# Kernel optimization log

Hardware: AMD Instinct MI355X
Metric: run time of the kernel (lower is better)

The kernel has to match this reference:

```python
import jax, jax.numpy as jnp
import numpy as np

N = 50000   # nodes
E = 200000  # triplets
IN = 128    # num_in_features
H = 4       # heads
F = 64      # num_out_features
HID = 64    # attention_mlp_hidden


def setup_inputs() -> dict:
    key = jax.random.key(0)
    ks = jax.random.split(key, 12)
    rn = lambda k, shape, s=0.05: (jax.random.normal(k, shape, jnp.float32) * s)
    return {
        "in_nodes_features": jax.random.normal(ks[0], (N, IN), jnp.float32),
        "edge_index": jax.random.randint(ks[1], (3, E), 0, N, jnp.int32),
        "W_proj": rn(ks[2], (H * F, IN)),          # linear_proj (no bias)
        "att_W1": rn(ks[3], (HID, 3 * F)),
        "att_b1": jnp.zeros((HID,), jnp.float32),
        "att_W2": rn(ks[4], (1, HID)),
        "att_b2": jnp.zeros((1,), jnp.float32),
        "e_W1": rn(ks[5], (F, 2 * F)),
        "e_b1": jnp.zeros((F,), jnp.float32),
        "e_W2": rn(ks[6], (F, F)),
        "e_b2": jnp.zeros((F,), jnp.float32),
        "theta": rn(ks[7], (1, H, F), 0.1),
        "bias": jnp.zeros((H * F,), jnp.float32),
    }


def _edge_nn(pair, e_W1, e_b1, e_W2, e_b2):
    # pair: [E, H, 2F] -> [E, H, F]
    h = jax.nn.leaky_relu(jnp.einsum('ehc,fc->ehf', pair, e_W1) + e_b1, 0.2)
    return jnp.einsum('ehf,gf->ehg', h, e_W2) + e_b2


def reference(in_nodes_features, edge_index, W_proj, att_W1, att_b1, att_W2,
              att_b2, e_W1, e_b1, e_W2, e_b2, theta, bias):
    proj = (in_nodes_features @ W_proj.T).reshape(-1, H, F)  # [N, H, F]
    pi = proj[edge_index[0]]  # [E, H, F]
    pj = proj[edge_index[1]]
    pk = proj[edge_index[2]]

    # attention MLP on concatenated triplet features
    comb = jnp.concatenate([pi, pj, pk], axis=-1)            # [E, H, 3F]
    h = jax.nn.relu(jnp.einsum('ehc,dc->ehd', comb, att_W1) + att_b1)
    scores = (jnp.einsum('ehd,od->eho', h, att_W2) + att_b2)[..., 0]  # [E, H]
    scores = jax.nn.leaky_relu(scores, 0.2)
    att = jax.nn.softmax(scores, axis=-1)[..., None]         # softmax over heads, [E, H, 1]

    pairs = [(pj, pk), (pi, pk), (pi, pj)]
    outs = []
    for i in range(3):
        prod = _edge_nn(jnp.concatenate(pairs[i], axis=-1), e_W1, e_b1, e_W2, e_b2)
        ws = jax.ops.segment_sum(att * prod, edge_index[i], num_segments=proj.shape[0])
        outs.append(theta * proj + ws)                       # [N, H, F]

    out = jnp.concatenate(outs, axis=0).reshape(-1, H * F)   # [3N, H*F]
    out = out + bias
    return jax.nn.elu(out)
```

## Files before the change

kernel.cpp:

```cpp
#include <hip/hip_runtime.h>
#include <hip/hip_bf16.h>

#define N_NODES 50000
#define N_EDGES 200000
#define IN_F 128
#define HEADS 4
#define FD 64
#define HF 256
#define NCOLS 1536
#define NT3 (3 * N_NODES)
#define E3  (3 * N_EDGES)
#define TROW 320

#define OFF_PROJ   0UL
#define OFF_TABS   51200000UL
#define OFF_ATT    179200000UL
#define OFF_RANK   182400000UL
#define OFF_ELIST2 184800000UL
#define OFF_CNT    194400000UL
#define OFF_OFFS   195000000UL
#define OFF_BSUM   195600008UL
#define OFF_BSW    195601040UL
#define OFF_CB     195994256UL

typedef __attribute__((ext_vector_type(8))) short short8;
typedef __attribute__((ext_vector_type(4))) float f32x4;

__device__ inline short bf16_of(float x) {
    __hip_bfloat16 h = __float2bfloat16(x);
    return *reinterpret_cast<short*>(&h);
}
__device__ inline unsigned pack2(float lo, float hi) {
    return ((unsigned)(unsigned short)bf16_of(hi) << 16) |
           (unsigned)(unsigned short)bf16_of(lo);
}
__device__ inline short8 pack8(float4 a, float4 b) {
    short8 o;
    o[0] = bf16_of(a.x); o[1] = bf16_of(a.y); o[2] = bf16_of(a.z); o[3] = bf16_of(a.w);
    o[4] = bf16_of(b.x); o[5] = bf16_of(b.y); o[6] = bf16_of(b.z); o[7] = bf16_of(b.w);
    return o;
}
__device__ inline void unpk(uint4 v, float* f) {
    f[0] = __uint_as_float(v.x << 16); f[1] = __uint_as_float(v.x & 0xffff0000u);
    f[2] = __uint_as_float(v.y << 16); f[3] = __uint_as_float(v.y & 0xffff0000u);
    f[4] = __uint_as_float(v.z << 16); f[5] = __uint_as_float(v.z & 0xffff0000u);
    f[6] = __uint_as_float(v.w << 16); f[7] = __uint_as_float(v.w & 0xffff0000u);
}
__device__ inline float score8(uint4 ua, uint4 ub, uint4 uc, const float* w) {
    float fa[8], fb[8], fc[8]; unpk(ua, fa); unpk(ub, fb); unpk(uc, fc);
    float p = 0.f;
#pragma unroll
    for (int j = 0; j < 8; ++j) {
        float x = fa[j] + fb[j] + fc[j];
        x = fmaxf(x, 0.f);
        p = fmaf(x, w[j], p);
    }
    return p;
}

__global__ __launch_bounds__(128) void k_comp(const float* __restrict__ Wp,
                                              const float* __restrict__ attW1,
                                              const float* __restrict__ eW1,
                                              const float* __restrict__ attb1,
                                              const float* __restrict__ eb1,
                                              __hip_bfloat16* __restrict__ Bsw,
                                              float* __restrict__ colbias) {
    const int c = blockIdx.x;
    const int k = threadIdx.x;
    float acc;
    float cb = 0.f;
    if (c < HF) {
        acc = Wp[c * IN_F + k];
    } else {
        const int t = (c - HF) >> 8;
        const int rem = (c - HF) & 255;
        const int h = rem >> 6, g = rem & 63;
        const float* T;
        if (t == 0)      T = attW1 + g * 192;
        else if (t == 1) T = attW1 + g * 192 + 64;
        else if (t == 2) T = attW1 + g * 192 + 128;
        else if (t == 3) T = eW1 + g * 128;
        else             T = eW1 + g * 128 + 64;
        acc = 0.f;
        for (int f = 0; f < 64; ++f)
            acc += T[f] * Wp[(h * 64 + f) * IN_F + k];
        if (t == 0) cb = attb1[g];
        else if (t == 3) cb = eb1[g];
    }
    const int ct = c >> 4, cin = c & 15, kin = k & 31, j = k & 7;
    const int ks = k >> 5;
    const int l = cin + ((kin >> 3) << 4);
    Bsw[((ct * 4 + ks) * 64 + l) * 8 + j] = __float2bfloat16(acc);
    if (k == 0) colbias[c] = cb;
}

__global__ __launch_bounds__(256) void k_tab(const float* __restrict__ in,
                                             const __hip_bfloat16* __restrict__ BswH,
                                             const float* __restrict__ colbias,
                                             float* __restrict__ proj,
                                             __hip_bfloat16* __restrict__ tabs) {
    const short8* Bsw = reinterpret_cast<const short8*>(BswH);
    const int lane = threadIdx.x & 63;
    const int wv = threadIdx.x >> 6;
    const int r = lane & 15, q = lane >> 4;
    const int row0 = blockIdx.x * 16;

    short8 a[4];
    const float* ip = in + (size_t)(row0 + r) * IN_F + q * 8;
#pragma unroll
    for (int ks = 0; ks < 4; ++ks)
        a[ks] = pack8(*(const float4*)(ip + ks * 32), *(const float4*)(ip + ks * 32 + 4));

    for (int ctl = 0; ctl < 24; ++ctl) {
        const int ct = wv * 24 + ctl;
        const int c = ct * 16 + r;
        const float cb = colbias[c];
        f32x4 acc = {cb, cb, cb, cb};
#pragma unroll
        for (int ks = 0; ks < 4; ++ks)
            acc = __builtin_amdgcn_mfma_f32_16x16x32_bf16(a[ks], Bsw[(ct * 4 + ks) * 64 + lane], acc, 0, 0, 0);
        if (c < HF) {
#pragma unroll
            for (int i = 0; i < 4; ++i)
                proj[(size_t)(row0 + q * 4 + i) * HF + c] = acc[i];
        } else {
            const int t = (c - HF) >> 8;
            const int rem = (c - HF) & 255;
            const int h = rem >> 6, g = rem & 63;
#pragma unroll
            for (int i = 0; i < 4; ++i)
                tabs[(((size_t)(row0 + q * 4 + i) * HEADS + h) * 5 + t) * 64 + g] =
                    __float2bfloat16(acc[i]);
        }
    }
}

__global__ __launch_bounds__(256) void k_hist(const int* __restrict__ eidx,
                                              int* __restrict__ cnt,
                                              int* __restrict__ rank) {
    const int g = blockIdx.x * 256 + threadIdx.x;
    if (g < E3) {
        const int node = eidx[g];
        const int t = g / N_EDGES;
        rank[g] = atomicAdd(&cnt[t * N_NODES + node], 1);
    }
}

__global__ __launch_bounds__(256) void k_scan1(const int* __restrict__ cnt,
                                               int* __restrict__ offs,
                                               int* __restrict__ bsums) {
    __shared__ int lds[256];
    const int b = blockIdx.x, t = threadIdx.x;
    const int base = b * 1024 + t * 4;
    int v[4];
#pragma unroll
    for (int c = 0; c < 4; ++c) v[c] = (base + c < NT3) ? cnt[base + c] : 0;
    const int s = v[0] + v[1] + v[2] + v[3];
    lds[t] = s;
    __syncthreads();
    for (int off = 1; off < 256; off <<= 1) {
        int x = (t >= off) ? lds[t - off] : 0;
        __syncthreads();
        lds[t] += x;
        __syncthreads();
    }
    if (t == 255) bsums[b] = lds[255];
    int run = lds[t] - s;
#pragma unroll
    for (int c = 0; c < 4; ++c) {
        if (base + c < NT3) offs[base + c] = run;
        run += v[c];
    }
}

__global__ __launch_bounds__(256) void k_scan2(int* __restrict__ bsums, int nb) {
    __shared__ int lds[256];
    const int t = threadIdx.x;
    const int v = (t < nb) ? bsums[t] : 0;
    lds[t] = v;
    __syncthreads();
    for (int off = 1; off < 256; off <<= 1) {
        int x = (t >= off) ? lds[t - off] : 0;
        __syncthreads();
        lds[t] += x;
        __syncthreads();
    }
    if (t < nb) bsums[t] = lds[t] - v;
}

__global__ __launch_bounds__(256) void k_scan3(int* __restrict__ offs,
                                               const int* __restrict__ bsums) {
    const int i = blockIdx.x * 256 + threadIdx.x;
    if (i < NT3) offs[i] += bsums[i >> 10];
    if (i == NT3) offs[NT3] = E3;
}

__global__ __launch_bounds__(256) void k_scat(const int* __restrict__ eidx,
                                              const int* __restrict__ offs,
                                              const int* __restrict__ rank,
                                              int4* __restrict__ elist2) {
    const int g = blockIdx.x * 256 + threadIdx.x;
    if (g < E3) {
        const int node = eidx[g];
        const int t = g / N_EDGES;
        const int e = g - t * N_EDGES;
        const int s0 = (t == 0) ? 1 : 0;
        const int s1 = (t == 2) ? 1 : 2;
        const int x = eidx[s0 * N_EDGES + e];
        const int y = eidx[s1 * N_EDGES + e];
        elist2[offs[t * N_NODES + node] + rank[g]] = make_int4(x, y, e, 0);
    }
}

__global__ __launch_bounds__(256) void k_att(
        const int* __restrict__ eidx,
        const __hip_bfloat16* __restrict__ tabs,
        const float* __restrict__ attW2, const float* __restrict__ attb2,
        float* __restrict__ attbuf) {
    __shared__ float s_lds[HEADS][16];
    const int lane = threadIdx.x & 63;
    const int h = threadIdx.x >> 6;
    const int r = lane & 15, q = lane >> 4;
    const int e0 = blockIdx.x * 16;

    float awlo[8], awhi[8];
    {
        float4 w0 = *(const float4*)(attW2 + q * 8);
        float4 w1 = *(const float4*)(attW2 + q * 8 + 4);
        awlo[0] = w0.x; awlo[1] = w0.y; awlo[2] = w0.z; awlo[3] = w0.w;
        awlo[4] = w1.x; awlo[5] = w1.y; awlo[6] = w1.z; awlo[7] = w1.w;
        float4 w2 = *(const float4*)(attW2 + 32 + q * 8);
        float4 w3 = *(const float4*)(attW2 + 32 + q * 8 + 4);
        awhi[0] = w2.x; awhi[1] = w2.y; awhi[2] = w2.z; awhi[3] = w2.w;
        awhi[4] = w3.x; awhi[5] = w3.y; awhi[6] = w3.z; awhi[7] = w3.w;
    }
    const float ab2s = attb2[0];

    const int ni = eidx[e0 + r];
    const int nj = eidx[N_EDGES + e0 + r];
    const int nk = eidx[2 * N_EDGES + e0 + r];

    const size_t bi = ((size_t)ni * HEADS + h) * TROW + q * 8;
    const size_t bj = ((size_t)nj * HEADS + h) * TROW + q * 8;
    const size_t bk = ((size_t)nk * HEADS + h) * TROW + q * 8;

    uint4 a0 = *(const uint4*)(tabs + bi);
    uint4 a1 = *(const uint4*)(tabs + bi + 32);
    uint4 b0 = *(const uint4*)(tabs + bj + 64);
    uint4 b1 = *(const uint4*)(tabs + bj + 96);
    uint4 c0 = *(const uint4*)(tabs + bk + 128);
    uint4 c1 = *(const uint4*)(tabs + bk + 160);

    float p = score8(a0, b0, c0, awlo) + score8(a1, b1, c1, awhi);
    p += __shfl_xor(p, 16);
    p += __shfl_xor(p, 32);
    float sc = p + ab2s;
    sc = fmaxf(sc, 0.2f * sc);
    if (lane < 16) s_lds[h][lane] = sc;
    __syncthreads();
    if (lane < 16) {
        const float s0 = s_lds[0][lane], s1 = s_lds[1][lane];
        const float s2 = s_lds[2][lane], s3 = s_lds[3][lane];
        const float mx = fmaxf(fmaxf(s0, s1), fmaxf(s2, s3));
        const float x0 = __expf(s0 - mx), x1 = __expf(s1 - mx);
        const float x2 = __expf(s2 - mx), x3 = __expf(s3 - mx);
        const float rs = 1.f / (x0 + x1 + x2 + x3);
        const float xh = (h == 0) ? x0 : (h == 1) ? x1 : (h == 2) ? x2 : x3;
        attbuf[(size_t)(e0 + lane) * 4 + h] = xh * rs;
    }
}

__global__ __launch_bounds__(256) void k_seg(const int* __restrict__ offs,
                                             const int4* __restrict__ elist2,
                                             const float* __restrict__ attbuf,
                                             const __hip_bfloat16* __restrict__ tabs,
                                             const float* __restrict__ proj,
                                             const float* __restrict__ eW2,
                                             const float* __restrict__ eb2,
                                             const float* __restrict__ theta,
                                             const float* __restrict__ bias,
                                             float* __restrict__ out) {
    __shared__ __hip_bfloat16 S_lds[16][72];
    __shared__ float a_lds[16];
    __shared__ float D_lds[16][68];

    const int lane = threadIdx.x & 63;
    const int w = threadIdx.x >> 6;
    const int h = lane >> 4, r = lane & 15;
    const int q = lane >> 4;
    const int t = blockIdx.y;
    const int n0 = blockIdx.x * 4;
    const int n = n0 + w;
    const int idx = t * N_NODES + n;
    const int p0 = offs[idx], p1 = offs[idx + 1];

    const int c1 = h * TROW + 192 + r * 4;
    const int c2 = h * TROW + 256 + r * 4;

    float acc0 = 0.f, acc1 = 0.f, acc2 = 0.f, acc3 = 0.f, alpha = 0.f;
    for (int base = p0; base < p1; base += 4) {
        int4 exy[4];
#pragma unroll
        for (int c = 0; c < 4; ++c) {
            const int p = base + c;
            exy[c] = elist2[p < p1 ? p : p1 - 1];
        }
        float at[4];
#pragma unroll
        for (int c = 0; c < 4; ++c)
            at[c] = (base + c < p1) ? attbuf[(size_t)exy[c].z * 4 + h] : 0.f;
        uint2 ua[4], ub[4];
#pragma unroll
        for (int c = 0; c < 4; ++c) {
            ua[c] = *(const uint2*)(tabs + ((size_t)exy[c].x * 1280 + c1));
            ub[c] = *(const uint2*)(tabs + ((size_t)exy[c].y * 1280 + c2));
        }
#pragma unroll
        for (int c = 0; c < 4; ++c) {
            float g0 = __uint_as_float(ua[c].x << 16) + __uint_as_float(ub[c].x << 16);
            float g1 = __uint_as_float(ua[c].x & 0xffff0000u) + __uint_as_float(ub[c].x & 0xffff0000u);
            float g2 = __uint_as_float(ua[c].y << 16) + __uint_as_float(ub[c].y << 16);
            float g3 = __uint_as_float(ua[c].y & 0xffff0000u) + __uint_as_float(ub[c].y & 0xffff0000u);
            g0 = fmaxf(g0, 0.2f * g0); g1 = fmaxf(g1, 0.2f * g1);
            g2 = fmaxf(g2, 0.2f * g2); g3 = fmaxf(g3, 0.2f * g3);
            acc0 = fmaf(at[c], g0, acc0); acc1 = fmaf(at[c], g1, acc1);
            acc2 = fmaf(at[c], g2, acc2); acc3 = fmaf(at[c], g3, acc3);
            alpha += at[c];
        }
    }
    const int tr = w * 4 + h;
    uint2 st;
    st.x = pack2(acc0, acc1);
    st.y = pack2(acc2, acc3);
    *(uint2*)&S_lds[tr][r * 4] = st;
    if (r == 0) a_lds[tr] = alpha;
    __syncthreads();

    {
        const float* wp0 = eW2 + (w * 16 + r) * FD + q * 8;
        const float* wp1 = eW2 + (w * 16 + r) * FD + 32 + q * 8;
        short8 bfr0 = pack8(*(const float4*)wp0, *(const float4*)(wp0 + 4));
        short8 bfr1 = pack8(*(const float4*)wp1, *(const float4*)(wp1 + 4));
        short8 A0 = *(short8*)&S_lds[r][q * 8];
        short8 A1 = *(short8*)&S_lds[r][32 + q * 8];
        f32x4 acc = {0.f, 0.f, 0.f, 0.f};
        acc = __builtin_amdgcn_mfma_f32_16x16x32_bf16(A0, bfr0, acc, 0, 0, 0);
        acc = __builtin_amdgcn_mfma_f32_16x16x32_bf16(A1, bfr1, acc, 0, 0, 0);
#pragma unroll
        for (int i = 0; i < 4; ++i)
            D_lds[q * 4 + i][w * 16 + r] = acc[i];
    }
    __syncthreads();

    const int row = threadIdx.x >> 4;
    const int c4 = threadIdx.x & 15;
    const int f = c4 * 4;
    const int hh = row & 3;
    const int nn = n0 + (row >> 2);
    const size_t rho = ((size_t)t * N_NODES + nn) * 4 + hh;

    float4 Dv = *(float4*)&D_lds[row][f];
    float4 pj = *(const float4*)(proj + (size_t)nn * HF + hh * 64 + f);
    float4 th = *(const float4*)(theta + hh * 64 + f);
    float4 bi = *(const float4*)(bias + hh * 64 + f);
    float4 b2 = *(const float4*)(eb2 + f);
    const float al = a_lds[row];
    float4 o;
    float v;
    v = th.x * pj.x + Dv.x + al * b2.x + bi.x; o.x = v > 0.f ? v : expm1f(v);
    v = th.y * pj.y + Dv.y + al * b2.y + bi.y; o.y = v > 0.f ? v : expm1f(v);
    v = th.z * pj.z + Dv.z + al * b2.z + bi.z; o.z = v > 0.f ? v : expm1f(v);
    v = th.w * pj.w + Dv.w + al * b2.w + bi.w; o.w = v > 0.f ? v : expm1f(v);
    *(float4*)(out + rho * 64 + f) = o;
}

extern "C" void kernel_launch(void* const* d_in, const int* in_sizes, int n_in,
                              void* d_out, int out_size, void* d_ws, size_t ws_size,
                              hipStream_t stream) {
    const float* in_nodes = (const float*)d_in[0];
    const int*   eidx     = (const int*)d_in[1];
    const float* Wp       = (const float*)d_in[2];
    const float* attW1    = (const float*)d_in[3];
    const float* attb1    = (const float*)d_in[4];
    const float* attW2    = (const float*)d_in[5];
    const float* attb2    = (const float*)d_in[6];
    const float* eW1      = (const float*)d_in[7];
    const float* eb1      = (const float*)d_in[8];
    const float* eW2      = (const float*)d_in[9];
    const float* eb2      = (const float*)d_in[10];
    const float* theta    = (const float*)d_in[11];
    const float* bias     = (const float*)d_in[12];

    char* ws = (char*)d_ws;
    float*          proj     = (float*)(ws + OFF_PROJ);
    __hip_bfloat16* tabs     = (__hip_bfloat16*)(ws + OFF_TABS);
    float*          attbuf   = (float*)(ws + OFF_ATT);
    int*            rank     = (int*)(ws + OFF_RANK);
    int4*           elist2   = (int4*)(ws + OFF_ELIST2);
    int*            cnt      = (int*)(ws + OFF_CNT);
    int*            offs     = (int*)(ws + OFF_OFFS);
    int*            bsums    = (int*)(ws + OFF_BSUM);
    __hip_bfloat16* Bsw      = (__hip_bfloat16*)(ws + OFF_BSW);
    float*          colbias  = (float*)(ws + OFF_CB);

    float* out = (float*)d_out;

    (void)hipMemsetAsync(cnt, 0, NT3 * sizeof(int), stream);

    k_comp<<<NCOLS, 128, 0, stream>>>(Wp, attW1, eW1, attb1, eb1, Bsw, colbias);
    k_tab<<<N_NODES / 16, 256, 0, stream>>>(in_nodes, Bsw, colbias, proj, tabs);

    k_hist<<<(E3 + 255) / 256, 256, 0, stream>>>(eidx, cnt, rank);
    k_scan1<<<(NT3 + 1023) / 1024, 256, 0, stream>>>(cnt, offs, bsums);
    k_scan2<<<1, 256, 0, stream>>>(bsums, (NT3 + 1023) / 1024);
    k_scan3<<<(NT3 + 256) / 256, 256, 0, stream>>>(offs, bsums);
    k_scat<<<(E3 + 255) / 256, 256, 0, stream>>>(eidx, offs, rank, elist2);

    k_att<<<N_EDGES / 16, 256, 0, stream>>>(eidx, tabs, attW2, attb2, attbuf);
    k_seg<<<dim3(N_NODES / 4, 3), 256, 0, stream>>>(offs, elist2, attbuf,
                                                    tabs, proj, eW2, eb2,
                                                    theta, bias, out);
}
```

Measured before the change: 366.6 us.

## Coalesce tab stores via LDS and process two nodes per wave in segment kernel

```diff
diff --git a/kernel.cpp b/kernel.cpp
--- a/kernel.cpp
+++ b/kernel.cpp
@@ -99,6 +99,7 @@
                                              const float* __restrict__ colbias,
                                              float* __restrict__ proj,
                                              __hip_bfloat16* __restrict__ tabs) {
+    __shared__ __hip_bfloat16 st_lds[4][16][20];
     const short8* Bsw = reinterpret_cast<const short8*>(BswH);
     const int lane = threadIdx.x & 63;
     const int wv = threadIdx.x >> 6;
@@ -124,13 +125,17 @@
             for (int i = 0; i < 4; ++i)
                 proj[(size_t)(row0 + q * 4 + i) * HF + c] = acc[i];
         } else {
-            const int t = (c - HF) >> 8;
-            const int rem = (c - HF) & 255;
-            const int h = rem >> 6, g = rem & 63;
 #pragma unroll
             for (int i = 0; i < 4; ++i)
-                tabs[(((size_t)(row0 + q * 4 + i) * HEADS + h) * 5 + t) * 64 + g] =
-                    __float2bfloat16(acc[i]);
+                st_lds[wv][q * 4 + i][r] = __float2bfloat16(acc[i]);
+            const int rem0 = ct * 16 - HF;
+            const int t = rem0 >> 8;
+            const int h = (rem0 >> 6) & 3;
+            const int g0 = rem0 & 63;
+            const int rowl = lane >> 2, ch = lane & 3;
+            uint2 val = *(const uint2*)&st_lds[wv][rowl][ch * 4];
+            *(uint2*)(tabs + ((size_t)(row0 + rowl) * 4 + h) * TROW +
+                      t * 64 + g0 + ch * 4) = val;
         }
     }
 }
@@ -280,60 +285,87 @@
                                              const float* __restrict__ theta,
                                              const float* __restrict__ bias,
                                              float* __restrict__ out) {
-    __shared__ __hip_bfloat16 S_lds[16][72];
-    __shared__ float a_lds[16];
-    __shared__ float D_lds[16][68];
+    __shared__ __hip_bfloat16 S_lds[2][16][72];
+    __shared__ float a_lds[2][16];
+    __shared__ float D_lds[2][16][68];
 
     const int lane = threadIdx.x & 63;
     const int w = threadIdx.x >> 6;
     const int h = lane >> 4, r = lane & 15;
     const int q = lane >> 4;
     const int t = blockIdx.y;
-    const int n0 = blockIdx.x * 4;
-    const int n = n0 + w;
-    const int idx = t * N_NODES + n;
-    const int p0 = offs[idx], p1 = offs[idx + 1];
+    const int n0 = blockIdx.x * 8;
+    const int idxA = t * N_NODES + n0 + w;
+    const int idxB = idxA + 4;
+    const int pA0 = offs[idxA], pA1 = offs[idxA + 1];
+    const int pB0 = offs[idxB], pB1 = offs[idxB + 1];
 
     const int c1 = h * TROW + 192 + r * 4;
     const int c2 = h * TROW + 256 + r * 4;
 
-    float acc0 = 0.f, acc1 = 0.f, acc2 = 0.f, acc3 = 0.f, alpha = 0.f;
-    for (int base = p0; base < p1; base += 4) {
-        int4 exy[4];
+    float aA0 = 0.f, aA1 = 0.f, aA2 = 0.f, aA3 = 0.f, alA = 0.f;
+    float aB0 = 0.f, aB1 = 0.f, aB2 = 0.f, aB3 = 0.f, alB = 0.f;
+    int baseA = pA0, baseB = pB0;
+    while (baseA < pA1 || baseB < pB1) {
+        int4 eA[4], eB[4];
 #pragma unroll
         for (int c = 0; c < 4; ++c) {
-            const int p = base + c;
-            exy[c] = elist2[p < p1 ? p : p1 - 1];
-        }
-        float at[4];
-#pragma unroll
-        for (int c = 0; c < 4; ++c)
-            at[c] = (base + c < p1) ? attbuf[(size_t)exy[c].z * 4 + h] : 0.f;
-        uint2 ua[4], ub[4];
+            int pa = baseA + c;
+            int ia = pa < pA1 ? pa : pA1 - 1; ia = ia < 0 ? 0 : ia;
+            eA[c] = elist2[ia];
+            int pb = baseB + c;
+            int ib = pb < pB1 ? pb : pB1 - 1; ib = ib < 0 ? 0 : ib;
+            eB[c] = elist2[ib];
+        }
+        float atA[4], atB[4];
 #pragma unroll
         for (int c = 0; c < 4; ++c) {
-            ua[c] = *(const uint2*)(tabs + ((size_t)exy[c].x * 1280 + c1));
-            ub[c] = *(const uint2*)(tabs + ((size_t)exy[c].y * 1280 + c2));
-        }
+            atA[c] = (baseA + c < pA1) ? attbuf[(size_t)eA[c].z * 4 + h] : 0.f;
+            atB[c] = (baseB + c < pB1) ? attbuf[(size_t)eB[c].z * 4 + h] : 0.f;
+        }
+        uint2 uaA[4], ubA[4], uaB[4], ubB[4];
 #pragma unroll
         for (int c = 0; c < 4; ++c) {
-            float g0 = __uint_as_float(ua[c].x << 16) + __uint_as_float(ub[c].x << 16);
-            float g1 = __uint_as_float(ua[c].x & 0xffff0000u) + __uint_as_float(ub[c].x & 0xffff0000u);
-            float g2 = __uint_as_float(ua[c].y << 16) + __uint_as_float(ub[c].y << 16);
-            float g3 = __uint_as_float(ua[c].y & 0xffff0000u) + __uint_as_float(ub[c].y & 0xffff0000u);
+            uaA[c] = *(const uint2*)(tabs + ((size_t)eA[c].x * 1280 + c1));
+            ubA[c] = *(const uint2*)(tabs + ((size_t)eA[c].y * 1280 + c2));
+            uaB[c] = *(const uint2*)(tabs + ((size_t)eB[c].x * 1280 + c1));
+            ubB[c] = *(const uint2*)(tabs + ((size_t)eB[c].y * 1280 + c2));
+        }
+#pragma unroll
+        for (int c = 0; c < 4; ++c) {
+            float g0 = __uint_as_float(uaA[c].x << 16) + __uint_as_float(ubA[c].x << 16);
+            float g1 = __uint_as_float(uaA[c].x & 0xffff0000u) + __uint_as_float(ubA[c].x & 0xffff0000u);
+            float g2 = __uint_as_float(uaA[c].y << 16) + __uint_as_float(ubA[c].y << 16);
+            float g3 = __uint_as_float(uaA[c].y & 0xffff0000u) + __uint_as_float(ubA[c].y & 0xffff0000u);
             g0 = fmaxf(g0, 0.2f * g0); g1 = fmaxf(g1, 0.2f * g1);
             g2 = fmaxf(g2, 0.2f * g2); g3 = fmaxf(g3, 0.2f * g3);
-            acc0 = fmaf(at[c], g0, acc0); acc1 = fmaf(at[c], g1, acc1);
-            acc2 = fmaf(at[c], g2, acc2); acc3 = fmaf(at[c], g3, acc3);
-            alpha += at[c];
-        }
+            aA0 = fmaf(atA[c], g0, aA0); aA1 = fmaf(atA[c], g1, aA1);
+            aA2 = fmaf(atA[c], g2, aA2); aA3 = fmaf(atA[c], g3, aA3);
+            alA += atA[c];
+        }
+#pragma unroll
+        for (int c = 0; c < 4; ++c) {
+            float g0 = __uint_as_float(uaB[c].x << 16) + __uint_as_float(ubB[c].x << 16);
+            float g1 = __uint_as_float(uaB[c].x & 0xffff0000u) + __uint_as_float(ubB[c].x & 0xffff0000u);
+            float g2 = __uint_as_float(uaB[c].y << 16) + __uint_as_float(ubB[c].y << 16);
+            float g3 = __uint_as_float(uaB[c].y & 0xffff0000u) + __uint_as_float(ubB[c].y & 0xffff0000u);
+            g0 = fmaxf(g0, 0.2f * g0); g1 = fmaxf(g1, 0.2f * g1);
+            g2 = fmaxf(g2, 0.2f * g2); g3 = fmaxf(g3, 0.2f * g3);
+            aB0 = fmaf(atB[c], g0, aB0); aB1 = fmaf(atB[c], g1, aB1);
+            aB2 = fmaf(atB[c], g2, aB2); aB3 = fmaf(atB[c], g3, aB3);
+            alB += atB[c];
+        }
+        baseA += 4; baseB += 4;
     }
     const int tr = w * 4 + h;
-    uint2 st;
-    st.x = pack2(acc0, acc1);
-    st.y = pack2(acc2, acc3);
-    *(uint2*)&S_lds[tr][r * 4] = st;
-    if (r == 0) a_lds[tr] = alpha;
+    {
+        uint2 st;
+        st.x = pack2(aA0, aA1); st.y = pack2(aA2, aA3);
+        *(uint2*)&S_lds[0][tr][r * 4] = st;
+        st.x = pack2(aB0, aB1); st.y = pack2(aB2, aB3);
+        *(uint2*)&S_lds[1][tr][r * 4] = st;
+        if (r == 0) { a_lds[0][tr] = alA; a_lds[1][tr] = alB; }
+    }
     __syncthreads();
 
     {
@@ -341,14 +373,17 @@
         const float* wp1 = eW2 + (w * 16 + r) * FD + 32 + q * 8;
         short8 bfr0 = pack8(*(const float4*)wp0, *(const float4*)(wp0 + 4));
         short8 bfr1 = pack8(*(const float4*)wp1, *(const float4*)(wp1 + 4));
-        short8 A0 = *(short8*)&S_lds[r][q * 8];
-        short8 A1 = *(short8*)&S_lds[r][32 + q * 8];
-        f32x4 acc = {0.f, 0.f, 0.f, 0.f};
-        acc = __builtin_amdgcn_mfma_f32_16x16x32_bf16(A0, bfr0, acc, 0, 0, 0);
-        acc = __builtin_amdgcn_mfma_f32_16x16x32_bf16(A1, bfr1, acc, 0, 0, 0);
-#pragma unroll
-        for (int i = 0; i < 4; ++i)
-            D_lds[q * 4 + i][w * 16 + r] = acc[i];
+#pragma unroll
+        for (int k = 0; k < 2; ++k) {
+            short8 A0 = *(short8*)&S_lds[k][r][q * 8];
+            short8 A1 = *(short8*)&S_lds[k][r][32 + q * 8];
+            f32x4 acc = {0.f, 0.f, 0.f, 0.f};
+            acc = __builtin_amdgcn_mfma_f32_16x16x32_bf16(A0, bfr0, acc, 0, 0, 0);
+            acc = __builtin_amdgcn_mfma_f32_16x16x32_bf16(A1, bfr1, acc, 0, 0, 0);
+#pragma unroll
+            for (int i = 0; i < 4; ++i)
+                D_lds[k][q * 4 + i][w * 16 + r] = acc[i];
+        }
     }
     __syncthreads();
 
@@ -356,22 +391,24 @@
     const int c4 = threadIdx.x & 15;
     const int f = c4 * 4;
     const int hh = row & 3;
-    const int nn = n0 + (row >> 2);
-    const size_t rho = ((size_t)t * N_NODES + nn) * 4 + hh;
-
-    float4 Dv = *(float4*)&D_lds[row][f];
-    float4 pj = *(const float4*)(proj + (size_t)nn * HF + hh * 64 + f);
     float4 th = *(const float4*)(theta + hh * 64 + f);
     float4 bi = *(const float4*)(bias + hh * 64 + f);
     float4 b2 = *(const float4*)(eb2 + f);
-    const float al = a_lds[row];
-    float4 o;
-    float v;
-    v = th.x * pj.x + Dv.x + al * b2.x + bi.x; o.x = v > 0.f ? v : expm1f(v);
-    v = th.y * pj.y + Dv.y + al * b2.y + bi.y; o.y = v > 0.f ? v : expm1f(v);
-    v = th.z * pj.z + Dv.z + al * b2.z + bi.z; o.z = v > 0.f ? v : expm1f(v);
-    v = th.w * pj.w + Dv.w + al * b2.w + bi.w; o.w = v > 0.f ? v : expm1f(v);
-    *(float4*)(out + rho * 64 + f) = o;
+#pragma unroll
+    for (int k = 0; k < 2; ++k) {
+        const int nn = n0 + k * 4 + (row >> 2);
+        const size_t rho = ((size_t)t * N_NODES + nn) * 4 + hh;
+        float4 Dv = *(float4*)&D_lds[k][row][f];
+        float4 pj = *(const float4*)(proj + (size_t)nn * HF + hh * 64 + f);
+        const float al = a_lds[k][row];
+        float4 o;
+        float v;
+        v = th.x * pj.x + Dv.x + al * b2.x + bi.x; o.x = v > 0.f ? v : expm1f(v);
+        v = th.y * pj.y + Dv.y + al * b2.y + bi.y; o.y = v > 0.f ? v : expm1f(v);
+        v = th.z * pj.z + Dv.z + al * b2.z + bi.z; o.z = v > 0.f ? v : expm1f(v);
+        v = th.w * pj.w + Dv.w + al * b2.w + bi.w; o.w = v > 0.f ? v : expm1f(v);
+        *(float4*)(out + rho * 64 + f) = o;
+    }
 }
 
 extern "C" void kernel_launch(void* const* d_in, const int* in_sizes, int n_in,
@@ -417,7 +454,7 @@
     k_scat<<<(E3 + 255) / 256, 256, 0, stream>>>(eidx, offs, rank, elist2);
 
     k_att<<<N_EDGES / 16, 256, 0, stream>>>(eidx, tabs, attW2, attb2, attbuf);
-    k_seg<<<dim3(N_NODES / 4, 3), 256, 0, stream>>>(offs, elist2, attbuf,
+    k_seg<<<dim3(N_NODES / 8, 3), 256, 0, stream>>>(offs, elist2, attbuf,
                                                     tabs, proj, eW2, eb2,
                                                     theta, bias, out);
 }
```

Measured after the change: 353.1 us. -3.7%, faster.
